# Performance work log

Hardware: AMD Instinct MI355X
Metric: run time of the kernel (lower is better)

## Reference

```python
import jax, jax.numpy as jnp
import numpy as np
from jax.scipy.linalg import expm

B, N, K = 2, 256, 16
ALPHA = 0.01       # prior anchoring weight
LAM = 1.0          # belief alignment weight
KAPPA = 1.0        # temperature
EPS = 1e-6
GCLIP = 1000.0     # grad_clip


def setup_inputs() -> dict:
    key = jax.random.key(0)
    ks = jax.random.split(key, 8)
    mu_q = jax.random.normal(ks[0], (B, N, K), dtype=jnp.float32)
    sigma_q = jax.random.uniform(ks[1], (B, N, K), dtype=jnp.float32, minval=0.1, maxval=1.0)
    mu_p = jax.random.normal(ks[2], (B, N, K), dtype=jnp.float32)
    sigma_p = jax.random.uniform(ks[3], (B, N, K), dtype=jnp.float32, minval=0.1, maxval=1.0)
    # beta: normalized attention weights over j (rows sum to 1)
    logits = jax.random.normal(ks[4], (B, N, N), dtype=jnp.float32)
    beta = jax.nn.softmax(logits, axis=-1)
    phi = 0.1 * jax.random.normal(ks[5], (B, N, 3), dtype=jnp.float32)
    # antisymmetric SO(3)-style generators (3, K, K)
    A = jax.random.normal(ks[6], (3, K, K), dtype=jnp.float32)
    generators = 0.5 * (A - jnp.swapaxes(A, -1, -2))
    lr = jnp.full((1,), 0.1, dtype=jnp.float32)
    return {"mu_q": mu_q, "sigma_q": sigma_q, "mu_p": mu_p, "sigma_p": sigma_p,
            "beta": beta, "phi": phi, "generators": generators, "lr": lr}


def _vfe_step(mu_q, sigma_q, mu_p, sigma_p, beta, phi, generators, lr):
    # ---- self-coupling KL(q||p) gradients (diagonal covariance) ----
    sigma_q_safe = jnp.clip(sigma_q, EPS)
    sigma_p_safe = jnp.clip(sigma_p, EPS)
    delta_mu = mu_q - mu_p
    grad_mu_self = ALPHA * delta_mu / sigma_p_safe                      # (B,N,K)
    grad_sigma_self = ALPHA * 0.5 * (1.0 / sigma_p_safe - 1.0 / sigma_q_safe)

    # ---- pairwise SO(3) gauge transport ----
    phi_matrix = jnp.einsum('bna,aij->bnij', phi, generators)           # (B,N,K,K)
    expm_b = jax.vmap(expm)
    exp_phi = expm_b(phi_matrix.reshape(B * N, K, K)).reshape(B, N, K, K)
    exp_neg_phi = expm_b((-phi_matrix).reshape(B * N, K, K)).reshape(B, N, K, K)
    Omega = jnp.einsum('bikl,bjlm->bijkm', exp_phi, exp_neg_phi)        # (B,N,N,K,K)

    mu_j_t = jnp.einsum('bijkl,bjl->bijk', Omega, mu_q)                 # (B,N,N,K)
    delta_ij = mu_q[:, :, None, :] - mu_j_t                             # (B,N,N,K)

    # Omega @ diag(sigma_j) @ Omega^T
    sigma_j_t = jnp.einsum('bijkl,bjl,bijml->bijkm', Omega, sigma_q_safe, Omega)
    eyeK = jnp.eye(K, dtype=mu_q.dtype)
    sigma_j_inv = jnp.linalg.inv(sigma_j_t + EPS * eyeK)                # (B,N,N,K,K)

    g = jnp.einsum('bijkl,bijl->bijk', sigma_j_inv, delta_ij)           # grad_kl_per_pair
    kl = 0.5 * jnp.einsum('bijk,bijk->bij', delta_ij, g)

    grad_mu_direct = LAM * jnp.einsum('bij,bijk->bik', beta, g)
    avg_grad = jnp.einsum('bij,bijk->bik', beta, g)
    grad_dev = g - avg_grad[:, :, None, :]
    d_beta = beta[..., None] * grad_dev / KAPPA
    grad_mu_soft = LAM * jnp.einsum('bij,bijk->bik', kl, d_beta)

    grad_mu = grad_mu_self + grad_mu_direct + grad_mu_soft
    grad_sigma = grad_sigma_self                                        # align term is zero for sigma

    # ---- natural gradient (Fisher metric, diagonal) ----
    nat_mu = sigma_q_safe * grad_mu
    nat_sigma = 0.5 * sigma_q_safe * sigma_q_safe * grad_sigma
    nat_mu = jnp.clip(nat_mu, -GCLIP, GCLIP)
    nat_sigma = jnp.clip(nat_sigma, -GCLIP, GCLIP)

    step = lr[0]
    mu_new = mu_q - step * nat_mu
    sigma_new = jnp.clip(sigma_q - step * nat_sigma, EPS)
    return jnp.stack([mu_new, sigma_new])                               # (2,B,N,K)


def reference(mu_q, sigma_q, mu_p, sigma_p, beta, phi, generators, lr):
    return _vfe_step(mu_q, sigma_q, mu_p, sigma_p, beta, phi, generators, lr)
```

## Files before the change

kernel.cpp:

```cpp
#include <hip/hip_runtime.h>
#include <hip/hip_fp16.h>

static constexpr int CB = 2;
static constexpr int CN = 256;
static constexpr int CK = 16;
static constexpr int NTRI = 136;
static constexpr int TS = 20;
#define F_ALPHA 0.01f
#define F_LAM   1.0f
#define F_KAPPA 1.0f
#define F_EPS   1e-6f
#define F_GCLIP 1000.0f

#define TRIOFF(r) ((r)*(33-(r))/2)

__global__ __launch_bounds__(256) void vfe_prep_kernel(
    const float* __restrict__ mu_q, const float* __restrict__ sigma_q,
    const float* __restrict__ phi, const float* __restrict__ gens,
    float* __restrict__ wsR, __half* __restrict__ wsWtriH, float* __restrict__ wsUT)
{
    const int bn = blockIdx.x;
    const int b  = bn >> 8;
    const int n  = bn & 255;
    const int t  = threadIdx.x;
    const int r  = t >> 4;
    const int c  = t & 15;

    __shared__ __align__(16) float Ms[256];
    __shared__ __align__(16) float Pa[256], Pb[256];
    __shared__ __align__(16) float Ta[256], Tb[256];
    __shared__ __align__(16) float TaT[16*TS], TbT[16*TS];
    __shared__ __align__(16) float Wst[256];
    __shared__ __align__(16) float msh[CK], dinv[CK];

    const float p0 = phi[bn*3+0];
    const float p1 = phi[bn*3+1];
    const float p2 = phi[bn*3+2];

    const float diag = (r == c) ? 1.0f : 0.0f;
    float m = p0*gens[t] + p1*gens[256+t] + p2*gens[512+t];
    m *= (1.0f/16.0f);
    Ms[t] = m;
    Pa[t] = m;
    if (t < CK) {
        msh[t]  = mu_q[bn*CK + t];
        dinv[t] = 1.0f / (fmaxf(sigma_q[bn*CK + t], F_EPS) + F_EPS);
    }
    __syncthreads();

    float mscol[CK];
    #pragma unroll
    for (int l = 0; l < CK; ++l) mscol[l] = Ms[l*CK + c];

    float Treg = diag + m;
    #pragma unroll
    for (int k = 2; k <= 8; ++k) {
        const float* Pc = (k & 1) ? Pb : Pa;
        float*       Pn = (k & 1) ? Pa : Pb;
        const float4* Pr = (const float4*)(Pc + r*CK);
        float acc = 0.f;
        #pragma unroll
        for (int q = 0; q < 4; ++q) {
            const float4 pv = Pr[q];
            acc += pv.x*mscol[4*q+0] + pv.y*mscol[4*q+1]
                 + pv.z*mscol[4*q+2] + pv.w*mscol[4*q+3];
        }
        acc *= (1.0f / (float)k);
        Pn[t] = acc;
        Treg += acc;
        __syncthreads();
    }

    Ta[t] = Treg;
    TaT[c*TS + r] = Treg;
    __syncthreads();
    #pragma unroll
    for (int s = 0; s < 4; ++s) {
        const float* Tc  = (s & 1) ? Tb  : Ta;
        const float* TcT = (s & 1) ? TbT : TaT;
        float*       Tn  = (s & 1) ? Ta  : Tb;
        float*       TnT = (s & 1) ? TaT : TbT;
        const float4* Rr = (const float4*)(Tc  + r*CK);
        const float4* Cc = (const float4*)(TcT + c*TS);
        float acc = 0.f;
        #pragma unroll
        for (int q = 0; q < 4; ++q) {
            const float4 a = Rr[q];
            const float4 bv = Cc[q];
            acc += a.x*bv.x + a.y*bv.y + a.z*bv.z + a.w*bv.w;
        }
        Tn[t] = acc;
        TnT[c*TS + r] = acc;
        __syncthreads();
    }

    if (t < CK) {
        const float4* Rt = (const float4*)(TaT + t*TS);
        const float4* mh = (const float4*)msh;
        float acc = 0.f;
        #pragma unroll
        for (int q = 0; q < 4; ++q) {
            const float4 a = Rt[q];
            const float4 mm = mh[q];
            acc += a.x*mm.x + a.y*mm.y + a.z*mm.z + a.w*mm.w;
        }
        wsUT[(b*CK + t)*CN + n] = acc;
    }

    if (t >= 64 && t < 128) {
        const int g = t - 64;
        float4 v;
        v.x = Ta[4*g+0]; v.y = Ta[4*g+1]; v.z = Ta[4*g+2]; v.w = Ta[4*g+3];
        ((float4*)wsR)[bn*64 + g] = v;
    }

    {
        const float4* Rr = (const float4*)(TaT + r*TS);
        const float4* Rc = (const float4*)(TaT + c*TS);
        const float4* dv = (const float4*)dinv;
        float acc = 0.f;
        #pragma unroll
        for (int q = 0; q < 4; ++q) {
            const float4 a = Rr[q];
            const float4 bb = Rc[q];
            const float4 dd = dv[q];
            acc += a.x*dd.x*bb.x + a.y*dd.y*bb.y + a.z*dd.z*bb.z + a.w*dd.w*bb.w;
        }
        Wst[t] = acc;
    }
    __syncthreads();

    if (t < NTRI) {
        int re = 0;
        #pragma unroll
        for (int q = 1; q < 16; ++q) re += (t >= TRIOFF(q));
        const int ce = t - TRIOFF(re) + re;
        wsWtriH[(b*NTRI + t)*CN + n] = __float2half_rn(Wst[re*CK + ce]);
    }
}

__global__ __launch_bounds__(256) void vfe_pair_kernel(
    const float* __restrict__ mu_q, const float* __restrict__ sigma_q,
    const float* __restrict__ mu_p, const float* __restrict__ sigma_p,
    const float* __restrict__ beta, const float* __restrict__ lr,
    const float* __restrict__ wsR, const __half* __restrict__ wsWtriH,
    const float* __restrict__ wsUT, float* __restrict__ out)
{
    const int bi = blockIdx.x;
    const int b  = bi >> 8;
    const int i  = bi & 255;
    const int t  = threadIdx.x;

    __shared__ float uish[CK];
    __shared__ float Hs[256][17];
    __shared__ float bets[256];
    __shared__ float bkls[256];
    __shared__ float partS1[4][16];
    __shared__ float partS2[4][16];
    __shared__ float partS3[4];
    __shared__ float grot[CK];

    if (t < CK) uish[t] = wsUT[(b*CK + t)*CN + i];
    __syncthreads();

    const float* uTb = wsUT + b*CK*CN;
    float d[CK];
    #pragma unroll
    for (int cc = 0; cc < CK; ++cc) d[cc] = uish[cc] - uTb[cc*CN + t];

    const __half* Wt = wsWtriH + (size_t)b*NTRI*CN + t;
    float h[CK];
    #pragma unroll
    for (int q = 0; q < CK; ++q) h[q] = 0.f;
    {
        int e = 0;
        #pragma unroll
        for (int rr = 0; rr < CK; ++rr) {
            #pragma unroll
            for (int cc = rr; cc < CK; ++cc) {
                const float w = __half2float(Wt[e*CN]);
                h[rr] += w * d[cc];
                if (cc > rr) h[cc] += w * d[rr];
                ++e;
            }
        }
    }
    float kl = 0.f;
    #pragma unroll
    for (int q = 0; q < CK; ++q) { Hs[t][q] = h[q]; kl += h[q]*d[q]; }
    kl *= 0.5f;

    const float bt = beta[(b*CN + i)*CN + t];
    bets[t] = bt;
    bkls[t] = bt * kl;
    __syncthreads();

    {
        const int k  = t & 15;
        const int jg = t >> 4;
        float s1p = 0.f, s2p = 0.f, s3p = 0.f;
        #pragma unroll
        for (int s = 0; s < 16; ++s) {
            const int jj = jg*16 + s;
            const float hv = Hs[jj][k];
            const float be = bets[jj];
            const float bk = bkls[jj];
            s1p += be * hv;
            s2p += bk * hv;
            s3p += bk;
        }
        s1p += __shfl_down(s1p, 16);  s1p += __shfl_down(s1p, 32);
        s2p += __shfl_down(s2p, 16);  s2p += __shfl_down(s2p, 32);
        s3p += __shfl_down(s3p, 16);  s3p += __shfl_down(s3p, 32);

        const int lane = t & 63;
        const int wv   = t >> 6;
        if (lane < 16) {
            partS1[wv][lane] = s1p;
            partS2[wv][lane] = s2p;
            if (lane == 0) partS3[wv] = s3p;
        }
    }
    __syncthreads();

    if (t < CK) {
        const float s1 = partS1[0][t] + partS1[1][t] + partS1[2][t] + partS1[3][t];
        const float s2 = partS2[0][t] + partS2[1][t] + partS2[2][t] + partS2[3][t];
        const float s3 = partS3[0] + partS3[1] + partS3[2] + partS3[3];
        grot[t] = F_LAM*s1 + (F_LAM/F_KAPPA)*(s2 - s3*s1);
    }
    __syncthreads();

    if (t < CK) {
        const int rr = t;
        const float* Ri = wsR + bi*256;
        float acc = 0.f;
        #pragma unroll
        for (int cc = 0; cc < CK; ++cc) acc += Ri[rr*CK+cc] * grot[cc];

        const int idx = bi*CK + rr;
        const float mq = mu_q[idx];
        const float sq = sigma_q[idx];
        const float mp = mu_p[idx];
        const float sp = sigma_p[idx];
        const float sps = fmaxf(sp, F_EPS);
        const float sqs = fmaxf(sq, F_EPS);

        const float gmu = F_ALPHA*(mq - mp)/sps + acc;
        const float gsg = F_ALPHA*0.5f*(1.0f/sps - 1.0f/sqs);

        float nmu = sqs * gmu;
        float nsg = 0.5f * sqs * sqs * gsg;
        nmu = fminf(fmaxf(nmu, -F_GCLIP), F_GCLIP);
        nsg = fminf(fmaxf(nsg, -F_GCLIP), F_GCLIP);

        const float step = lr[0];
        out[idx]             = mq - step*nmu;
        out[CB*CN*CK + idx]  = fmaxf(sq - step*nsg, F_EPS);
    }
}

extern "C" void kernel_launch(void* const* d_in, const int* in_sizes, int n_in,
                              void* d_out, int out_size, void* d_ws, size_t ws_size,
                              hipStream_t stream) {
    const float* mu_q    = (const float*)d_in[0];
    const float* sigma_q = (const float*)d_in[1];
    const float* mu_p    = (const float*)d_in[2];
    const float* sigma_p = (const float*)d_in[3];
    const float* beta    = (const float*)d_in[4];
    const float* phi     = (const float*)d_in[5];
    const float* gens    = (const float*)d_in[6];
    const float* lr      = (const float*)d_in[7];
    float* out = (float*)d_out;

    float*  wsR     = (float*)d_ws;
    __half* wsWtriH = (__half*)(wsR + CB*CN*CK*CK);
    float*  wsUT    = (float*)((char*)wsWtriH + ((CB*NTRI*CN*sizeof(__half) + 15) & ~15));

    vfe_prep_kernel<<<CB*CN, 256, 0, stream>>>(mu_q, sigma_q, phi, gens,
                                               wsR, wsWtriH, wsUT);
    vfe_pair_kernel<<<CB*CN, 256, 0, stream>>>(mu_q, sigma_q, mu_p, sigma_p, beta, lr,
                                               wsR, wsWtriH, wsUT, out);
}
```

Measured before the change: 16.02 us.

## Store full fp16 W matrix packed and use fdot2; shorten expm series

The pair kernel now reads the full 16x16 fp16 weight matrix as packed uint4 rows and computes each h entry with packed-half dot products (fdot2). This replaces the scalar symmetric-triangle loop with its separate half loads and conversions. The prep kernel also changes the scaling-and-squaring setup: scale by 1/8 with a Taylor series to order 6 and 3 squarings, instead of 1/16 with order 8 and 4 squarings. This trades some accuracy in the matrix exponential and in the fp16 quantisation of the d vector for less compute and wider loads, at the cost of reading about twice as much W data as the triangular layout.

```diff
diff --git a/kernel.cpp b/kernel.cpp
--- a/kernel.cpp
+++ b/kernel.cpp
@@ -4,7 +4,6 @@
 static constexpr int CB = 2;
 static constexpr int CN = 256;
 static constexpr int CK = 16;
-static constexpr int NTRI = 136;
 static constexpr int TS = 20;
 #define F_ALPHA 0.01f
 #define F_LAM   1.0f
@@ -12,12 +11,19 @@
 #define F_EPS   1e-6f
 #define F_GCLIP 1000.0f
 
-#define TRIOFF(r) ((r)*(33-(r))/2)
+typedef _Float16 h2_t __attribute__((ext_vector_type(2)));
+__device__ inline h2_t as_h2(unsigned u) { union { unsigned u; h2_t h; } x; x.u = u; return x.h; }
+
+#if __has_builtin(__builtin_amdgcn_fdot2)
+#define FDOT2(a, b, c) __builtin_amdgcn_fdot2((a), (b), (c), false)
+#else
+#define FDOT2(a, b, c) ((c) + (float)(a).x * (float)(b).x + (float)(a).y * (float)(b).y)
+#endif
 
 __global__ __launch_bounds__(256) void vfe_prep_kernel(
     const float* __restrict__ mu_q, const float* __restrict__ sigma_q,
     const float* __restrict__ phi, const float* __restrict__ gens,
-    float* __restrict__ wsR, __half* __restrict__ wsWtriH, float* __restrict__ wsUT)
+    float* __restrict__ wsR, unsigned* __restrict__ wsW16, float* __restrict__ wsUT)
 {
     const int bn = blockIdx.x;
     const int b  = bn >> 8;
@@ -39,7 +45,7 @@
 
     const float diag = (r == c) ? 1.0f : 0.0f;
     float m = p0*gens[t] + p1*gens[256+t] + p2*gens[512+t];
-    m *= (1.0f/16.0f);
+    m *= (1.0f/8.0f);
     Ms[t] = m;
     Pa[t] = m;
     if (t < CK) {
@@ -54,7 +60,7 @@
 
     float Treg = diag + m;
     #pragma unroll
-    for (int k = 2; k <= 8; ++k) {
+    for (int k = 2; k <= 6; ++k) {
         const float* Pc = (k & 1) ? Pb : Pa;
         float*       Pn = (k & 1) ? Pa : Pb;
         const float4* Pr = (const float4*)(Pc + r*CK);
@@ -75,7 +81,7 @@
     TaT[c*TS + r] = Treg;
     __syncthreads();
     #pragma unroll
-    for (int s = 0; s < 4; ++s) {
+    for (int s = 0; s < 3; ++s) {
         const float* Tc  = (s & 1) ? Tb  : Ta;
         const float* TcT = (s & 1) ? TbT : TaT;
         float*       Tn  = (s & 1) ? Ta  : Tb;
@@ -95,7 +101,7 @@
     }
 
     if (t < CK) {
-        const float4* Rt = (const float4*)(TaT + t*TS);
+        const float4* Rt = (const float4*)(TbT + t*TS);
         const float4* mh = (const float4*)msh;
         float acc = 0.f;
         #pragma unroll
@@ -110,13 +116,13 @@
     if (t >= 64 && t < 128) {
         const int g = t - 64;
         float4 v;
-        v.x = Ta[4*g+0]; v.y = Ta[4*g+1]; v.z = Ta[4*g+2]; v.w = Ta[4*g+3];
+        v.x = Tb[4*g+0]; v.y = Tb[4*g+1]; v.z = Tb[4*g+2]; v.w = Tb[4*g+3];
         ((float4*)wsR)[bn*64 + g] = v;
     }
 
     {
-        const float4* Rr = (const float4*)(TaT + r*TS);
-        const float4* Rc = (const float4*)(TaT + c*TS);
+        const float4* Rr = (const float4*)(TbT + r*TS);
+        const float4* Rc = (const float4*)(TbT + c*TS);
         const float4* dv = (const float4*)dinv;
         float acc = 0.f;
         #pragma unroll
@@ -130,12 +136,16 @@
     }
     __syncthreads();
 
-    if (t < NTRI) {
-        int re = 0;
-        #pragma unroll
-        for (int q = 1; q < 16; ++q) re += (t >= TRIOFF(q));
-        const int ce = t - TRIOFF(re) + re;
-        wsWtriH[(b*NTRI + t)*CN + n] = __float2half_rn(Wst[re*CK + ce]);
+    if (t < 32) {
+        const int g = t;
+        unsigned pk[4];
+        #pragma unroll
+        for (int q = 0; q < 4; ++q) {
+            __half2 p = __floats2half2_rn(Wst[g*8 + 2*q], Wst[g*8 + 2*q + 1]);
+            pk[q] = *reinterpret_cast<unsigned*>(&p);
+        }
+        uint4 v; v.x = pk[0]; v.y = pk[1]; v.z = pk[2]; v.w = pk[3];
+        ((uint4*)wsW16)[(size_t)(b*32 + g)*CN + n] = v;
     }
 }
 
@@ -143,7 +153,7 @@
     const float* __restrict__ mu_q, const float* __restrict__ sigma_q,
     const float* __restrict__ mu_p, const float* __restrict__ sigma_p,
     const float* __restrict__ beta, const float* __restrict__ lr,
-    const float* __restrict__ wsR, const __half* __restrict__ wsWtriH,
+    const float* __restrict__ wsR, const unsigned* __restrict__ wsW16,
     const float* __restrict__ wsUT, float* __restrict__ out)
 {
     const int bi = blockIdx.x;
@@ -168,26 +178,33 @@
     #pragma unroll
     for (int cc = 0; cc < CK; ++cc) d[cc] = uish[cc] - uTb[cc*CN + t];
 
-    const __half* Wt = wsWtriH + (size_t)b*NTRI*CN + t;
+    h2_t dh[8];
+    #pragma unroll
+    for (int q = 0; q < 8; ++q) {
+        h2_t v; v.x = (_Float16)d[2*q]; v.y = (_Float16)d[2*q+1];
+        dh[q] = v;
+    }
+
+    const uint4* Wb = ((const uint4*)wsW16) + (size_t)b*32*CN + t;
     float h[CK];
-    #pragma unroll
-    for (int q = 0; q < CK; ++q) h[q] = 0.f;
-    {
-        int e = 0;
-        #pragma unroll
-        for (int rr = 0; rr < CK; ++rr) {
-            #pragma unroll
-            for (int cc = rr; cc < CK; ++cc) {
-                const float w = __half2float(Wt[e*CN]);
-                h[rr] += w * d[cc];
-                if (cc > rr) h[cc] += w * d[rr];
-                ++e;
-            }
-        }
-    }
     float kl = 0.f;
     #pragma unroll
-    for (int q = 0; q < CK; ++q) { Hs[t][q] = h[q]; kl += h[q]*d[q]; }
+    for (int rr = 0; rr < CK; ++rr) {
+        const uint4 w0 = Wb[(size_t)(rr*2    )*CN];
+        const uint4 w1 = Wb[(size_t)(rr*2 + 1)*CN];
+        float acc = 0.f;
+        acc = FDOT2(as_h2(w0.x), dh[0], acc);
+        acc = FDOT2(as_h2(w0.y), dh[1], acc);
+        acc = FDOT2(as_h2(w0.z), dh[2], acc);
+        acc = FDOT2(as_h2(w0.w), dh[3], acc);
+        acc = FDOT2(as_h2(w1.x), dh[4], acc);
+        acc = FDOT2(as_h2(w1.y), dh[5], acc);
+        acc = FDOT2(as_h2(w1.z), dh[6], acc);
+        acc = FDOT2(as_h2(w1.w), dh[7], acc);
+        h[rr] = acc;
+        Hs[t][rr] = acc;
+        kl += acc * d[rr];
+    }
     kl *= 0.5f;
 
     const float bt = beta[(b*CN + i)*CN + t];
@@ -273,12 +290,12 @@
     const float* lr      = (const float*)d_in[7];
     float* out = (float*)d_out;
 
-    float*  wsR     = (float*)d_ws;
-    __half* wsWtriH = (__half*)(wsR + CB*CN*CK*CK);
-    float*  wsUT    = (float*)((char*)wsWtriH + ((CB*NTRI*CN*sizeof(__half) + 15) & ~15));
+    float*    wsR   = (float*)d_ws;
+    unsigned* wsW16 = (unsigned*)(wsR + CB*CN*CK*CK);
+    float*    wsUT  = (float*)((char*)wsW16 + (size_t)CB*32*CN*16);
 
     vfe_prep_kernel<<<CB*CN, 256, 0, stream>>>(mu_q, sigma_q, phi, gens,
-                                               wsR, wsWtriH, wsUT);
+                                               wsR, wsW16, wsUT);
     vfe_pair_kernel<<<CB*CN, 256, 0, stream>>>(mu_q, sigma_q, mu_p, sigma_p, beta, lr,
-                                               wsR, wsWtriH, wsUT, out);
+                                               wsR, wsW16, wsUT, out);
 }
```

New measurement: 15.45 us. 1.04x faster.
